# Performance work log

Measured on AMD Instinct MI355X. Metric: run time of the kernel, lower is better.

## Reference

```python
import jax, jax.numpy as jnp
import numpy as np

D_MODEL = 1024
NUM_HEAD = 16
D_HEAD = 64
SEQ = 1024
MEM = 1024
BATCH = 4
LN_EPS = 1e-5


def _rel_shift(x):
    # x: [i, j, b, n] -- Transformer-XL relative shift trick
    i, j, b, n = x.shape
    zero_pad = jnp.zeros((i, 1, b, n), dtype=x.dtype)
    x_padded = jnp.concatenate([zero_pad, x], axis=1).reshape(j + 1, i, b, n)
    return x_padded[1:].reshape(i, j, b, n)


def setup_inputs() -> dict:
    key = jax.random.key(0)
    ks = jax.random.split(key, 8)
    w_scale = 1.0 / np.sqrt(D_MODEL)  # keep activations O(1)
    total = MEM + SEQ
    return {
        "x": jax.random.normal(ks[0], (SEQ, BATCH, D_MODEL), jnp.float32),
        "memory": jax.random.normal(ks[1], (MEM, BATCH, D_MODEL), jnp.float32),
        "pos_emb": jax.random.normal(ks[2], (total, BATCH, D_MODEL), jnp.float32),
        "pos_bias_u": jax.random.normal(ks[3], (NUM_HEAD, D_HEAD), jnp.float32) * 0.02,
        "pos_bias_v": jax.random.normal(ks[4], (NUM_HEAD, D_HEAD), jnp.float32) * 0.02,
        "W_qkv": jax.random.normal(ks[5], (3 * NUM_HEAD * D_HEAD, D_MODEL), jnp.float32) * w_scale,
        "W_rel": jax.random.normal(ks[6], (NUM_HEAD * D_HEAD, D_MODEL), jnp.float32) * w_scale,
        "W_o": jax.random.normal(ks[7], (D_MODEL, NUM_HEAD * D_HEAD), jnp.float32) * w_scale,
        "ln_gamma": jnp.ones((D_MODEL,), jnp.float32),
        "ln_beta": jnp.zeros((D_MODEL,), jnp.float32),
    }


def reference(x, memory, pos_emb, pos_bias_u, pos_bias_v, W_qkv, W_rel, W_o, ln_gamma, ln_beta):
    seq_len = x.shape[0]
    c = jnp.concatenate([memory, x], axis=0)        # [T, B, D]
    T, B = c.shape[0], c.shape[1]
    n, d = pos_bias_u.shape
    scale = 1.0 / np.sqrt(d)

    heads = c @ W_qkv.T                              # [T, B, 3*n*d]
    q, k, v = jnp.split(heads, 3, axis=-1)
    q = q.reshape(T, B, n, d)[-seq_len:]             # [S, B, n, d]
    k = k.reshape(T, B, n, d)                        # [T, B, n, d]
    v = v.reshape(T, B, n, d)
    r = (pos_emb @ W_rel.T).reshape(T, B, n, d)      # [T, B, n, d]

    AC = jnp.einsum('ibnd,jbnd->ijbn', q + pos_bias_u, k)
    BD = _rel_shift(jnp.einsum('ibnd,jbnd->ijbn', q + pos_bias_v, r))
    attn_score = (AC + BD) * scale                   # [S, T, B, n]
    attn_prob = jax.nn.softmax(attn_score, axis=1)   # softmax over key dim (dropout = eval identity)

    attn_vec = jnp.einsum('ijbn,jbnd->ibnd', attn_prob, v).reshape(seq_len, B, n * d)
    attn_out = attn_vec @ W_o.T                      # [S, B, D]

    y = x + attn_out
    mu = jnp.mean(y, axis=-1, keepdims=True)
    var = jnp.mean(jnp.square(y - mu), axis=-1, keepdims=True)
    return ln_gamma * (y - mu) / jnp.sqrt(var + LN_EPS) + ln_beta
```

## Files before the change

kernel.cpp:

```cpp
#include <hip/hip_runtime.h>

#define S_ 1024
#define M_ 1024
#define T_ 2048
#define B_ 4
#define H_ 16
#define DM_ 1024
#define DH_ 64

typedef __attribute__((ext_vector_type(8))) short s16x8;
typedef __attribute__((ext_vector_type(16))) float f32x16;

__device__ __forceinline__ unsigned short f2b(float x){
  unsigned int u = __float_as_uint(x);
  u = (u + 0x7fffu + ((u>>16)&1u)) >> 16;
  return (unsigned short)u;
}
__device__ __forceinline__ float b2f(unsigned short h){
  return __uint_as_float(((unsigned int)h)<<16);
}
__device__ __forceinline__ uint4 pack8(const float* v){
  uint4 o;
  o.x = (unsigned)f2b(v[0]) | ((unsigned)f2b(v[1])<<16);
  o.y = (unsigned)f2b(v[2]) | ((unsigned)f2b(v[3])<<16);
  o.z = (unsigned)f2b(v[4]) | ((unsigned)f2b(v[5])<<16);
  o.w = (unsigned)f2b(v[6]) | ((unsigned)f2b(v[7])<<16);
  return o;
}
__device__ __forceinline__ void glds16(const unsigned short* g, unsigned short* l){
  __builtin_amdgcn_global_load_lds((const __attribute__((address_space(1))) void*)g,
                                   (__attribute__((address_space(3))) void*)l, 16, 0, 0);
}

__global__ __launch_bounds__(256) void cast_cat(const float* __restrict__ a,
    const float* __restrict__ b, unsigned short* __restrict__ dst, int n8, int na8)
{
  int i = blockIdx.x*256 + threadIdx.x;
  if (i >= n8) return;
  const float* src = (i < na8) ? (a + (size_t)i*8) : (b + ((size_t)(i-na8))*8);
  float4 x0 = *(const float4*)src;
  float4 x1 = *(const float4*)(src+4);
  float f[8] = {x0.x,x0.y,x0.z,x0.w,x1.x,x1.y,x1.z,x1.w};
  *(uint4*)&dst[(size_t)i*8] = pack8(f);
}

__global__ __launch_bounds__(256) void gemm_nt(const unsigned short* __restrict__ A,
    const unsigned short* __restrict__ Bw, void* __restrict__ Cout,
    const float* __restrict__ res, int Ntot, int K, int mode)
{
  __shared__ __align__(16) unsigned short a_s[128*64];
  __shared__ __align__(16) unsigned short b_s[128*64];
  const int tid = threadIdx.x;
  const int lane = tid & 63, wave = tid >> 6;
  const int wr = wave >> 1, wc = wave & 1;
  const long m0 = (long)blockIdx.y * 128, n0 = (long)blockIdx.x * 128;
  f32x16 acc[2][2];
  for (int qa=0;qa<2;qa++) for(int qb=0;qb<2;qb++) for (int e=0;e<16;e++) acc[qa][qb][e]=0.f;
  int srow[4], scol[4];
  for (int c = 0; c < 4; c++) {
    int ch = c*256 + tid;
    srow[c] = ch >> 3;
    scol[c] = (((ch & 7) ^ (srow[c] & 7))) * 8;
  }
  for (int k0 = 0; k0 < K; k0 += 64) {
    for (int c = 0; c < 4; c++) {
      int ch = c*256 + tid;
      glds16(&A[(size_t)(m0+srow[c])*K + k0 + scol[c]], &a_s[ch*8]);
      glds16(&Bw[(size_t)(n0+srow[c])*K + k0 + scol[c]], &b_s[ch*8]);
    }
    __syncthreads();
    for (int ks = 0; ks < 4; ks++) {
      const int kb = ks*2 + (lane>>5);
      s16x8 af[2], bf[2];
      for (int q = 0; q < 2; q++) {
        int ra = wr*64 + q*32 + (lane&31);
        int rb = wc*64 + q*32 + (lane&31);
        af[q] = *(const s16x8*)&a_s[ra*64 + ((kb ^ (ra&7))<<3)];
        bf[q] = *(const s16x8*)&b_s[rb*64 + ((kb ^ (rb&7))<<3)];
      }
      for (int qr=0;qr<2;qr++)
        for (int qc2=0;qc2<2;qc2++)
          acc[qr][qc2] = __builtin_amdgcn_mfma_f32_32x32x16_bf16(af[qr], bf[qc2], acc[qr][qc2], 0,0,0);
    }
    __syncthreads();
  }
  for (int qr=0;qr<2;qr++)
    for (int qc2=0;qc2<2;qc2++)
      for (int e=0;e<16;e++){
        long row = m0 + wr*64 + qr*32 + (e&3) + 8*(e>>2) + 4*(lane>>5);
        long col = n0 + wc*64 + qc2*32 + (lane&31);
        size_t o = (size_t)row*Ntot + col;
        if (mode == 0) ((unsigned short*)Cout)[o] = f2b(acc[qr][qc2][e]);
        else           ((float*)Cout)[o] = acc[qr][qc2][e] + res[o];
      }
}

__global__ __launch_bounds__(256) void scatter_quv(const unsigned short* __restrict__ qkvo,
   const float* __restrict__ u, const float* __restrict__ v,
   unsigned short* __restrict__ QU, unsigned short* __restrict__ QV)
{
  int gid = blockIdx.x*256 + threadIdx.x;
  int d0 = (gid & 7) * 8;
  int i  = (gid >> 3) & (S_-1);
  int bh = gid >> 13;
  int b = bh >> 4, h = bh & 15;
  size_t src = (size_t)((M_+i)*B_ + b)*3072 + h*64 + d0;
  uint4 q8 = *(const uint4*)&qkvo[src];
  float f[8];
  f[0]=b2f(q8.x&0xffff); f[1]=b2f(q8.x>>16); f[2]=b2f(q8.y&0xffff); f[3]=b2f(q8.y>>16);
  f[4]=b2f(q8.z&0xffff); f[5]=b2f(q8.z>>16); f[6]=b2f(q8.w&0xffff); f[7]=b2f(q8.w>>16);
  float fu[8], fv[8];
  for (int e=0;e<8;e++){ fu[e] = f[e] + u[h*64+d0+e]; fv[e] = f[e] + v[h*64+d0+e]; }
  size_t dst = ((size_t)bh*S_ + i)*64 + d0;
  *(uint4*)&QU[dst] = pack8(fu);
  *(uint4*)&QV[dst] = pack8(fv);
}

__global__ __launch_bounds__(256) void scatter_vt(const unsigned short* __restrict__ qkvo,
    unsigned short* __restrict__ VT)
{
  __shared__ __align__(16) unsigned short v_s[64*72];
  const int tid = threadIdx.x;
  const int bh = blockIdx.x, b = bh>>4, h = bh&15;
  const int t0 = blockIdx.y*64;
  const unsigned short* Vg = qkvo + (size_t)b*3072 + 2048 + h*64;
  for (int c=0;c<2;c++){
    int ch = c*256 + tid;
    int r = ch>>3, off = (ch&7)*8;
    *(uint4*)&v_s[r*72+off] = *(const uint4*)&Vg[(size_t)(t0+r)*12288 + off];
  }
  __syncthreads();
  for (int c=0;c<2;c++){
    int ch = c*256 + tid;
    int d = ch>>3, toff = (ch&7)*8;
    unsigned short vals[8];
    for (int e=0;e<8;e++) vals[e] = v_s[(toff+e)*72 + d];
    uint4 pk;
    pk.x = (unsigned)vals[0] | ((unsigned)vals[1]<<16);
    pk.y = (unsigned)vals[2] | ((unsigned)vals[3]<<16);
    pk.z = (unsigned)vals[4] | ((unsigned)vals[5]<<16);
    pk.w = (unsigned)vals[6] | ((unsigned)vals[7]<<16);
    *(uint4*)&VT[((size_t)bh*64 + d)*T_ + t0 + toff] = pk;
  }
}

__global__ __launch_bounds__(256,2) void flash_attn4(
    const unsigned short* __restrict__ QU, const unsigned short* __restrict__ QV,
    const unsigned short* __restrict__ qkvo, const unsigned short* __restrict__ VT,
    const unsigned short* __restrict__ relo, unsigned short* __restrict__ AV)
{
  __shared__ __align__(16) unsigned short qu_s[64*72];
  __shared__ __align__(16) unsigned short qv_s[65*72];
  __shared__ __align__(16) unsigned short k_s [64*72];
  __shared__ __align__(16) unsigned short vT_s[64*72];
  __shared__ __align__(16) unsigned short r_s [128*64];
  __shared__ __align__(16) unsigned short g_s [64*128];
  __shared__ __align__(16) unsigned short p_s [64*72];
  __shared__ float l_s[64];

  const int tid = threadIdx.x, lane = tid&63, wave = tid>>6;
  const int bh = blockIdx.x, b = bh>>4, h = bh&15;
  const int i0 = blockIdx.y*64;
  const int qr = wave>>1, qc = wave&1;
  const unsigned short* QUb = QU + (size_t)bh*S_*DH_;
  const unsigned short* QVb = QV + (size_t)bh*S_*DH_;
  const unsigned short* Kg  = qkvo + (size_t)b*3072 + 1024 + h*64;
  const unsigned short* VTb = VT + (size_t)bh*64*T_;
  const unsigned short* Rg  = relo + (size_t)b*1024 + h*64;

  for (int c=0;c<2;c++){
    int ch = c*256+tid; int row = ch>>3, off=(ch&7)*8;
    *(uint4*)&qu_s[row*72+off] = *(const uint4*)&QUb[(size_t)(i0+row)*64 + off];
    *(uint4*)&qv_s[row*72+off] = *(const uint4*)&QVb[(size_t)(i0+row)*64 + off];
  }
  if (tid < 8) {
    int rr = i0 + 64; if (rr > S_-1) rr = S_-1;
    *(uint4*)&qv_s[64*72 + tid*8] = *(const uint4*)&QVb[(size_t)rr*64 + tid*8];
  }

  f32x16 acc_o;
  for (int e=0;e<16;e++) acc_o[e]=0.f;
  float lreg = 0.f;

  const int col = qc*32 + (lane&31);
  int rowl[16];
  for (int e=0;e<16;e++) rowl[e] = qr*32 + (e&3) + 8*(e>>2) + 4*(lane>>5);

  for (int j0 = 0; j0 < T_; j0 += 64) {
    const int jdmax = j0 + 63 - i0;
    const int jdmin = j0 - 63 - i0;
    const int cls = (jdmax <= 1024) ? 0 : ((jdmin >= 1026) ? 2 : 1);
    const int wb = (cls == 2) ? (j0 - i0 - 1089) : (j0 - i0 + 960);
    const int ashift = (cls == 2) ? 1 : 0;

    for (int c=0;c<2;c++){
      int ch = c*256+tid; int row = ch>>3, off=(ch&7)*8;
      *(uint4*)&k_s[row*72+off]  = *(const uint4*)&Kg[(size_t)(j0+row)*12288 + off];
      *(uint4*)&vT_s[row*72+off] = *(const uint4*)&VTb[(size_t)row*T_ + j0 + off];
    }
    for (int c=0;c<4;c++){
      int ch = c*256+tid; int rr = ch>>3, off = ch&7;
      int t = wb + rr; t = t < 0 ? 0 : (t > T_-1 ? T_-1 : t);
      *(uint4*)&r_s[rr*64 + ((off ^ (rr&7))<<3)] = *(const uint4*)&Rg[(size_t)t*4096 + off*8];
    }
    __syncthreads();

    for (int qi=0; qi<2; qi++){
      int qq = qc*2 + qi;
      f32x16 gacc;
      for (int e=0;e<16;e++) gacc[e]=0.f;
      for (int ks=0; ks<4; ks++){
        int koff = ks*16 + (lane>>5)*8, kb = ks*2 + (lane>>5);
        int ar = qr*32 + (lane&31) + ashift;
        int br = qq*32 + (lane&31);
        s16x8 a  = *(const s16x8*)&qv_s[ar*72 + koff];
        s16x8 bb = *(const s16x8*)&r_s[br*64 + ((kb ^ (br&7))<<3)];
        gacc = __builtin_amdgcn_mfma_f32_32x32x16_bf16(a, bb, gacc, 0,0,0);
      }
      for (int e=0;e<16;e++){
        int r = qr*32 + (e&3) + 8*(e>>2) + 4*(lane>>5);
        g_s[r*128 + qq*32 + (lane&31)] = f2b(gacc[e]);
      }
    }
    f32x16 acc;
    for (int e=0;e<16;e++) acc[e]=0.f;
    for (int ks=0; ks<4; ks++){
      int koff = ks*16 + (lane>>5)*8;
      s16x8 a  = *(const s16x8*)&qu_s[(qr*32+(lane&31))*72 + koff];
      s16x8 bq = *(const s16x8*)&k_s[(qc*32+(lane&31))*72 + koff];
      acc = __builtin_amdgcn_mfma_f32_32x32x16_bf16(a, bq, acc, 0,0,0);
    }
    __syncthreads();

    for (int e=0;e<16;e++){
      int r = rowl[e];
      int jd = j0 + col - (i0 + r);
      if (cls == 1 && jd >= 1026) continue;
      float bd = (jd == 1025) ? 0.f : b2f(g_s[r*128 + (col - r + 63)]);
      p_s[r*72 + col] = f2b(__expf((acc[e] + bd) * 0.125f));
    }
    if (cls == 1) {
      __syncthreads();
      const int wb2 = j0 - i0 - 1089;
      for (int c=0;c<4;c++){
        int ch = c*256+tid; int rr = ch>>3, off = ch&7;
        int t = wb2 + rr; t = t < 0 ? 0 : (t > T_-1 ? T_-1 : t);
        *(uint4*)&r_s[rr*64 + ((off ^ (rr&7))<<3)] = *(const uint4*)&Rg[(size_t)t*4096 + off*8];
      }
      __syncthreads();
      for (int qi=0; qi<2; qi++){
        int qq = qc*2 + qi;
        f32x16 gacc;
        for (int e=0;e<16;e++) gacc[e]=0.f;
        for (int ks=0; ks<4; ks++){
          int koff = ks*16 + (lane>>5)*8, kb = ks*2 + (lane>>5);
          int ar = qr*32 + (lane&31) + 1;
          int br = qq*32 + (lane&31);
          s16x8 a  = *(const s16x8*)&qv_s[ar*72 + koff];
          s16x8 bb = *(const s16x8*)&r_s[br*64 + ((kb ^ (br&7))<<3)];
          gacc = __builtin_amdgcn_mfma_f32_32x32x16_bf16(a, bb, gacc, 0,0,0);
        }
        for (int e=0;e<16;e++){
          int r = qr*32 + (e&3) + 8*(e>>2) + 4*(lane>>5);
          g_s[r*128 + qq*32 + (lane&31)] = f2b(gacc[e]);
        }
      }
      __syncthreads();
      for (int e=0;e<16;e++){
        int r = rowl[e];
        int jd = j0 + col - (i0 + r);
        if (jd < 1026) continue;
        float bd = b2f(g_s[r*128 + (col - r + 63)]);
        p_s[r*72 + col] = f2b(__expf((acc[e] + bd) * 0.125f));
      }
    }
    __syncthreads();

    {
      int rr = tid>>2, cb = (tid&3)*16;
      uint4 x0 = *(const uint4*)&p_s[rr*72+cb];
      uint4 x1 = *(const uint4*)&p_s[rr*72+cb+8];
      unsigned vs[8] = {x0.x,x0.y,x0.z,x0.w,x1.x,x1.y,x1.z,x1.w};
      float s = 0.f;
      for (int e=0;e<8;e++) s += b2f((unsigned short)(vs[e]&0xffff)) + b2f((unsigned short)(vs[e]>>16));
      s += __shfl_xor(s, 1, 64);
      s += __shfl_xor(s, 2, 64);
      if ((tid&3)==0) lreg += s;
    }
    for (int ks=0; ks<4; ks++){
      int koff = ks*16 + (lane>>5)*8;
      s16x8 a  = *(const s16x8*)&p_s[(qr*32+(lane&31))*72 + koff];
      s16x8 bv = *(const s16x8*)&vT_s[(qc*32+(lane&31))*72 + koff];
      acc_o = __builtin_amdgcn_mfma_f32_32x32x16_bf16(a, bv, acc_o, 0,0,0);
    }
    __syncthreads();
  }

  if ((tid&3)==0) l_s[tid>>2] = lreg;
  __syncthreads();
  for (int e=0;e<16;e++){
    float oo = acc_o[e] / l_s[rowl[e]];
    AV[ ((size_t)(i0+rowl[e])*B_ + b)*(H_*DH_) + h*DH_ + col ] = f2b(oo);
  }
}

__global__ __launch_bounds__(256) void ln_kernel(const float* __restrict__ y,
    const float* __restrict__ g, const float* __restrict__ be, float* __restrict__ o)
{
  __shared__ float red[8];
  int row = blockIdx.x, tid = threadIdx.x;
  const float* yr = y + (size_t)row*DM_;
  float v[4];
  for (int e=0;e<4;e++) v[e] = yr[tid + 256*e];
  float s = v[0]+v[1]+v[2]+v[3];
  for (int off=32; off>0; off>>=1) s += __shfl_down(s, off, 64);
  if ((tid&63)==0) red[tid>>6] = s;
  __syncthreads();
  if (tid==0) red[4] = red[0]+red[1]+red[2]+red[3];
  __syncthreads();
  float mu = red[4] * (1.f/DM_);
  __syncthreads();
  float q = 0.f;
  for (int e=0;e<4;e++){ float d = v[e]-mu; q += d*d; }
  for (int off=32; off>0; off>>=1) q += __shfl_down(q, off, 64);
  if ((tid&63)==0) red[tid>>6] = q;
  __syncthreads();
  if (tid==0) red[4] = red[0]+red[1]+red[2]+red[3];
  __syncthreads();
  float rstd = rsqrtf(red[4]*(1.f/DM_) + 1e-5f);
  for (int e=0;e<4;e++){
    int c = tid + 256*e;
    o[(size_t)row*DM_ + c] = g[c]*(v[e]-mu)*rstd + be[c];
  }
}

extern "C" void kernel_launch(void* const* d_in, const int* in_sizes, int n_in,
                              void* d_out, int out_size, void* d_ws, size_t ws_size,
                              hipStream_t stream)
{
  const float* x    = (const float*)d_in[0];
  const float* mem  = (const float*)d_in[1];
  const float* pos  = (const float*)d_in[2];
  const float* pbu  = (const float*)d_in[3];
  const float* pbv  = (const float*)d_in[4];
  const float* wqkv = (const float*)d_in[5];
  const float* wrel = (const float*)d_in[6];
  const float* wo   = (const float*)d_in[7];
  const float* gam  = (const float*)d_in[8];
  const float* bet  = (const float*)d_in[9];
  float* out = (float*)d_out;

  char* w = (char*)d_ws;
  unsigned short* qkvo  = (unsigned short*)(w + 0);
  unsigned short* relo  = (unsigned short*)(w + 50331648);
  unsigned short* wo16  = (unsigned short*)(w + 67108864);
  unsigned short* QUb   = (unsigned short*)(w + 69206016);
  unsigned short* QVb   = (unsigned short*)(w + 77594624);
  unsigned short* VT    = (unsigned short*)(w + 85983232);
  unsigned short* av16  = (unsigned short*)(w + 102760448);
  float*          yf    = (float*)(w + 111149056);
  unsigned short* c16   = (unsigned short*)(w + 127926272);
  unsigned short* pos16 = (unsigned short*)(w + 144703488);
  unsigned short* wq16  = (unsigned short*)(w + 161480704);
  unsigned short* wr16  = (unsigned short*)(w + 167772160);

  cast_cat<<<4096, 256, 0, stream>>>(mem, x, c16, 1048576, 524288);
  cast_cat<<<4096, 256, 0, stream>>>(pos, pos, pos16, 1048576, 1048576);
  cast_cat<<<1536, 256, 0, stream>>>(wqkv, wqkv, wq16, 393216, 393216);
  cast_cat<<< 512, 256, 0, stream>>>(wrel, wrel, wr16, 131072, 131072);
  cast_cat<<< 512, 256, 0, stream>>>(wo,   wo,   wo16, 131072, 131072);

  gemm_nt<<<dim3(24,64), 256, 0, stream>>>(c16,   wq16, (void*)qkvo, nullptr, 3072, 1024, 0);
  gemm_nt<<<dim3(8,64),  256, 0, stream>>>(pos16, wr16, (void*)relo, nullptr, 1024, 1024, 0);

  scatter_quv<<<2048, 256, 0, stream>>>(qkvo, pbu, pbv, QUb, QVb);
  scatter_vt<<<dim3(64,32), 256, 0, stream>>>(qkvo, VT);

  flash_attn4<<<dim3(64,16), 256, 0, stream>>>(QUb, QVb, qkvo, VT, relo, av16);

  gemm_nt<<<dim3(8,32), 256, 0, stream>>>(av16, wo16, (void*)yf, x, 1024, 1024, 1);
  ln_kernel<<<4096, 256, 0, stream>>>(yf, gam, bet, out);
}
```

Before: 532.4 us.

## Prefetch next K/V/R tiles into registers and alias LDS buffers for occupancy

```diff
diff --git a/kernel.cpp b/kernel.cpp
--- a/kernel.cpp
+++ b/kernel.cpp
@@ -144,18 +144,16 @@
   }
 }
 
-__global__ __launch_bounds__(256,2) void flash_attn4(
+__global__ __launch_bounds__(256,3) void flash_attn4(
     const unsigned short* __restrict__ QU, const unsigned short* __restrict__ QV,
     const unsigned short* __restrict__ qkvo, const unsigned short* __restrict__ VT,
     const unsigned short* __restrict__ relo, unsigned short* __restrict__ AV)
 {
   __shared__ __align__(16) unsigned short qu_s[64*72];
   __shared__ __align__(16) unsigned short qv_s[65*72];
-  __shared__ __align__(16) unsigned short k_s [64*72];
+  __shared__ __align__(16) unsigned short kp_s[64*72];
   __shared__ __align__(16) unsigned short vT_s[64*72];
-  __shared__ __align__(16) unsigned short r_s [128*64];
-  __shared__ __align__(16) unsigned short g_s [64*128];
-  __shared__ __align__(16) unsigned short p_s [64*72];
+  __shared__ __align__(16) unsigned short rg_s[64*128];
   __shared__ float l_s[64];
 
   const int tid = threadIdx.x, lane = tid&63, wave = tid>>6;
@@ -183,43 +181,66 @@
   float lreg = 0.f;
 
   const int col = qc*32 + (lane&31);
-  int rowl[16];
-  for (int e=0;e<16;e++) rowl[e] = qr*32 + (e&3) + 8*(e>>2) + 4*(lane>>5);
+  const int rbase = qr*32 + 4*(lane>>5);
+
+  uint4 pk0, pk1, pv0, pv1, pr0, pr1, pr2, pr3;
+  const int r0c = tid>>3,        o0c = (tid&7)*8;
+  const int r1c = (256+tid)>>3,  o1c = ((256+tid)&7)*8;
+
+#define PREF(J) do { \
+    pk0 = *(const uint4*)&Kg [(size_t)((J)+r0c)*12288 + o0c]; \
+    pk1 = *(const uint4*)&Kg [(size_t)((J)+r1c)*12288 + o1c]; \
+    pv0 = *(const uint4*)&VTb[(size_t)r0c*T_ + (J) + o0c];    \
+    pv1 = *(const uint4*)&VTb[(size_t)r1c*T_ + (J) + o1c];    \
+    int jdmax_ = (J)+63-i0, jdmin_ = (J)-63-i0;               \
+    int cls_ = (jdmax_<=1024)?0:((jdmin_>=1026)?2:1);         \
+    int wb_ = (cls_==2)?((J)-i0-1089):((J)-i0+960);           \
+    { int rr_=(0*256+tid)>>3; int t_=wb_+rr_; t_=t_<0?0:(t_>T_-1?T_-1:t_); pr0=*(const uint4*)&Rg[(size_t)t_*4096 + ((0*256+tid)&7)*8]; } \
+    { int rr_=(1*256+tid)>>3; int t_=wb_+rr_; t_=t_<0?0:(t_>T_-1?T_-1:t_); pr1=*(const uint4*)&Rg[(size_t)t_*4096 + ((1*256+tid)&7)*8]; } \
+    { int rr_=(2*256+tid)>>3; int t_=wb_+rr_; t_=t_<0?0:(t_>T_-1?T_-1:t_); pr2=*(const uint4*)&Rg[(size_t)t_*4096 + ((2*256+tid)&7)*8]; } \
+    { int rr_=(3*256+tid)>>3; int t_=wb_+rr_; t_=t_<0?0:(t_>T_-1?T_-1:t_); pr3=*(const uint4*)&Rg[(size_t)t_*4096 + ((3*256+tid)&7)*8]; } \
+  } while(0)
+
+#define STORE_STAGE() do { \
+    *(uint4*)&kp_s[r0c*72+o0c] = pk0; \
+    *(uint4*)&kp_s[r1c*72+o1c] = pk1; \
+    *(uint4*)&vT_s[r0c*72+o0c] = pv0; \
+    *(uint4*)&vT_s[r1c*72+o1c] = pv1; \
+    { int rr_=(0*256+tid)>>3, of_=(0*256+tid)&7; *(uint4*)&rg_s[rr_*64 + ((of_^(rr_&7))<<3)] = pr0; } \
+    { int rr_=(1*256+tid)>>3, of_=(1*256+tid)&7; *(uint4*)&rg_s[rr_*64 + ((of_^(rr_&7))<<3)] = pr1; } \
+    { int rr_=(2*256+tid)>>3, of_=(2*256+tid)&7; *(uint4*)&rg_s[rr_*64 + ((of_^(rr_&7))<<3)] = pr2; } \
+    { int rr_=(3*256+tid)>>3, of_=(3*256+tid)&7; *(uint4*)&rg_s[rr_*64 + ((of_^(rr_&7))<<3)] = pr3; } \
+  } while(0)
+
+  PREF(0);
 
   for (int j0 = 0; j0 < T_; j0 += 64) {
     const int jdmax = j0 + 63 - i0;
     const int jdmin = j0 - 63 - i0;
     const int cls = (jdmax <= 1024) ? 0 : ((jdmin >= 1026) ? 2 : 1);
-    const int wb = (cls == 2) ? (j0 - i0 - 1089) : (j0 - i0 + 960);
     const int ashift = (cls == 2) ? 1 : 0;
 
-    for (int c=0;c<2;c++){
-      int ch = c*256+tid; int row = ch>>3, off=(ch&7)*8;
-      *(uint4*)&k_s[row*72+off]  = *(const uint4*)&Kg[(size_t)(j0+row)*12288 + off];
-      *(uint4*)&vT_s[row*72+off] = *(const uint4*)&VTb[(size_t)row*T_ + j0 + off];
-    }
-    for (int c=0;c<4;c++){
-      int ch = c*256+tid; int rr = ch>>3, off = ch&7;
-      int t = wb + rr; t = t < 0 ? 0 : (t > T_-1 ? T_-1 : t);
-      *(uint4*)&r_s[rr*64 + ((off ^ (rr&7))<<3)] = *(const uint4*)&Rg[(size_t)t*4096 + off*8];
-    }
-    __syncthreads();
-
-    for (int qi=0; qi<2; qi++){
-      int qq = qc*2 + qi;
-      f32x16 gacc;
-      for (int e=0;e<16;e++) gacc[e]=0.f;
-      for (int ks=0; ks<4; ks++){
-        int koff = ks*16 + (lane>>5)*8, kb = ks*2 + (lane>>5);
-        int ar = qr*32 + (lane&31) + ashift;
-        int br = qq*32 + (lane&31);
-        s16x8 a  = *(const s16x8*)&qv_s[ar*72 + koff];
-        s16x8 bb = *(const s16x8*)&r_s[br*64 + ((kb ^ (br&7))<<3)];
-        gacc = __builtin_amdgcn_mfma_f32_32x32x16_bf16(a, bb, gacc, 0,0,0);
-      }
-      for (int e=0;e<16;e++){
-        int r = qr*32 + (e&3) + 8*(e>>2) + 4*(lane>>5);
-        g_s[r*128 + qq*32 + (lane&31)] = f2b(gacc[e]);
+    STORE_STAGE();
+    __syncthreads();
+
+    if (j0 + 64 < T_) PREF(j0 + 64);
+
+    f32x16 gacc0, gacc1;
+    for (int e=0;e<16;e++){ gacc0[e]=0.f; gacc1[e]=0.f; }
+    __builtin_amdgcn_s_setprio(1);
+    for (int ks=0; ks<4; ks++){
+      int koff = ks*16 + (lane>>5)*8, kb = ks*2 + (lane>>5);
+      int ar = qr*32 + (lane&31) + ashift;
+      s16x8 a  = *(const s16x8*)&qv_s[ar*72 + koff];
+      {
+        int br = (qc*2+0)*32 + (lane&31);
+        s16x8 bb = *(const s16x8*)&rg_s[br*64 + ((kb ^ (br&7))<<3)];
+        gacc0 = __builtin_amdgcn_mfma_f32_32x32x16_bf16(a, bb, gacc0, 0,0,0);
+      }
+      {
+        int br = (qc*2+1)*32 + (lane&31);
+        s16x8 bb = *(const s16x8*)&rg_s[br*64 + ((kb ^ (br&7))<<3)];
+        gacc1 = __builtin_amdgcn_mfma_f32_32x32x16_bf16(a, bb, gacc1, 0,0,0);
       }
     }
     f32x16 acc;
@@ -227,17 +248,25 @@
     for (int ks=0; ks<4; ks++){
       int koff = ks*16 + (lane>>5)*8;
       s16x8 a  = *(const s16x8*)&qu_s[(qr*32+(lane&31))*72 + koff];
-      s16x8 bq = *(const s16x8*)&k_s[(qc*32+(lane&31))*72 + koff];
+      s16x8 bq = *(const s16x8*)&kp_s[(qc*32+(lane&31))*72 + koff];
       acc = __builtin_amdgcn_mfma_f32_32x32x16_bf16(a, bq, acc, 0,0,0);
     }
+    __builtin_amdgcn_s_setprio(0);
     __syncthreads();
 
     for (int e=0;e<16;e++){
-      int r = rowl[e];
+      int r = rbase + (e&3) + 8*(e>>2);
+      rg_s[r*128 + (qc*2+0)*32 + (lane&31)] = f2b(gacc0[e]);
+      rg_s[r*128 + (qc*2+1)*32 + (lane&31)] = f2b(gacc1[e]);
+    }
+    __syncthreads();
+
+    for (int e=0;e<16;e++){
+      int r = rbase + (e&3) + 8*(e>>2);
       int jd = j0 + col - (i0 + r);
       if (cls == 1 && jd >= 1026) continue;
-      float bd = (jd == 1025) ? 0.f : b2f(g_s[r*128 + (col - r + 63)]);
-      p_s[r*72 + col] = f2b(__expf((acc[e] + bd) * 0.125f));
+      float bd = (jd == 1025) ? 0.f : b2f(rg_s[r*128 + (col - r + 63)]);
+      kp_s[r*72 + col] = f2b(__expf((acc[e] + bd) * 0.125f));
     }
     if (cls == 1) {
       __syncthreads();
@@ -245,41 +274,49 @@
       for (int c=0;c<4;c++){
         int ch = c*256+tid; int rr = ch>>3, off = ch&7;
         int t = wb2 + rr; t = t < 0 ? 0 : (t > T_-1 ? T_-1 : t);
-        *(uint4*)&r_s[rr*64 + ((off ^ (rr&7))<<3)] = *(const uint4*)&Rg[(size_t)t*4096 + off*8];
+        *(uint4*)&rg_s[rr*64 + ((off ^ (rr&7))<<3)] = *(const uint4*)&Rg[(size_t)t*4096 + off*8];
       }
       __syncthreads();
-      for (int qi=0; qi<2; qi++){
-        int qq = qc*2 + qi;
-        f32x16 gacc;
-        for (int e=0;e<16;e++) gacc[e]=0.f;
-        for (int ks=0; ks<4; ks++){
-          int koff = ks*16 + (lane>>5)*8, kb = ks*2 + (lane>>5);
-          int ar = qr*32 + (lane&31) + 1;
-          int br = qq*32 + (lane&31);
-          s16x8 a  = *(const s16x8*)&qv_s[ar*72 + koff];
-          s16x8 bb = *(const s16x8*)&r_s[br*64 + ((kb ^ (br&7))<<3)];
-          gacc = __builtin_amdgcn_mfma_f32_32x32x16_bf16(a, bb, gacc, 0,0,0);
+      f32x16 g2a, g2b;
+      for (int e=0;e<16;e++){ g2a[e]=0.f; g2b[e]=0.f; }
+      __builtin_amdgcn_s_setprio(1);
+      for (int ks=0; ks<4; ks++){
+        int koff = ks*16 + (lane>>5)*8, kb = ks*2 + (lane>>5);
+        int ar = qr*32 + (lane&31) + 1;
+        s16x8 a  = *(const s16x8*)&qv_s[ar*72 + koff];
+        {
+          int br = (qc*2+0)*32 + (lane&31);
+          s16x8 bb = *(const s16x8*)&rg_s[br*64 + ((kb ^ (br&7))<<3)];
+          g2a = __builtin_amdgcn_mfma_f32_32x32x16_bf16(a, bb, g2a, 0,0,0);
         }
-        for (int e=0;e<16;e++){
-          int r = qr*32 + (e&3) + 8*(e>>2) + 4*(lane>>5);
-          g_s[r*128 + qq*32 + (lane&31)] = f2b(gacc[e]);
+        {
+          int br = (qc*2+1)*32 + (lane&31);
+          s16x8 bb = *(const s16x8*)&rg_s[br*64 + ((kb ^ (br&7))<<3)];
+          g2b = __builtin_amdgcn_mfma_f32_32x32x16_bf16(a, bb, g2b, 0,0,0);
         }
       }
+      __builtin_amdgcn_s_setprio(0);
       __syncthreads();
       for (int e=0;e<16;e++){
-        int r = rowl[e];
+        int r = rbase + (e&3) + 8*(e>>2);
+        rg_s[r*128 + (qc*2+0)*32 + (lane&31)] = f2b(g2a[e]);
+        rg_s[r*128 + (qc*2+1)*32 + (lane&31)] = f2b(g2b[e]);
+      }
+      __syncthreads();
+      for (int e=0;e<16;e++){
+        int r = rbase + (e&3) + 8*(e>>2);
         int jd = j0 + col - (i0 + r);
         if (jd < 1026) continue;
-        float bd = b2f(g_s[r*128 + (col - r + 63)]);
-        p_s[r*72 + col] = f2b(__expf((acc[e] + bd) * 0.125f));
+        float bd = b2f(rg_s[r*128 + (col - r + 63)]);
+        kp_s[r*72 + col] = f2b(__expf((acc[e] + bd) * 0.125f));
       }
     }
     __syncthreads();
 
     {
       int rr = tid>>2, cb = (tid&3)*16;
-      uint4 x0 = *(const uint4*)&p_s[rr*72+cb];
-      uint4 x1 = *(const uint4*)&p_s[rr*72+cb+8];
+      uint4 x0 = *(const uint4*)&kp_s[rr*72+cb];
+      uint4 x1 = *(const uint4*)&kp_s[rr*72+cb+8];
       unsigned vs[8] = {x0.x,x0.y,x0.z,x0.w,x1.x,x1.y,x1.z,x1.w};
       float s = 0.f;
       for (int e=0;e<8;e++) s += b2f((unsigned short)(vs[e]&0xffff)) + b2f((unsigned short)(vs[e]>>16));
@@ -287,21 +324,26 @@
       s += __shfl_xor(s, 2, 64);
       if ((tid&3)==0) lreg += s;
     }
+    __builtin_amdgcn_s_setprio(1);
     for (int ks=0; ks<4; ks++){
       int koff = ks*16 + (lane>>5)*8;
-      s16x8 a  = *(const s16x8*)&p_s[(qr*32+(lane&31))*72 + koff];
+      s16x8 a  = *(const s16x8*)&kp_s[(qr*32+(lane&31))*72 + koff];
       s16x8 bv = *(const s16x8*)&vT_s[(qc*32+(lane&31))*72 + koff];
       acc_o = __builtin_amdgcn_mfma_f32_32x32x16_bf16(a, bv, acc_o, 0,0,0);
     }
+    __builtin_amdgcn_s_setprio(0);
     __syncthreads();
   }
 
   if ((tid&3)==0) l_s[tid>>2] = lreg;
   __syncthreads();
   for (int e=0;e<16;e++){
-    float oo = acc_o[e] / l_s[rowl[e]];
-    AV[ ((size_t)(i0+rowl[e])*B_ + b)*(H_*DH_) + h*DH_ + col ] = f2b(oo);
-  }
+    int r = rbase + (e&3) + 8*(e>>2);
+    float oo = acc_o[e] / l_s[r];
+    AV[ ((size_t)(i0+r)*B_ + b)*(H_*DH_) + h*DH_ + col ] = f2b(oo);
+  }
+#undef PREF
+#undef STORE_STAGE
 }
 
 __global__ __launch_bounds__(256) void ln_kernel(const float* __restrict__ y,
```

New measurement: 1.032 ms. 1.94x slower.
